# Performance work log

Measured on AMD Instinct MI355X. Metric: run time of the kernel, lower is better.

The kernel has to match this reference:

```python
import jax, jax.numpy as jnp
import numpy as np

B, T, C = 1, 2048, 2048
H = 16
DN, DR, DV = 128, 64, 128          # qk_nope_head_dim, qk_rope_head_dim, v_head_dim
QKD = DN + DR                      # 192
RQ, RKV = 1536, 512                # q_lora_rank, kv_lora_rank
EPS = 1e-6
SCALE = QKD ** -0.5


def rmsnorm(v, w):
    return v * jax.lax.rsqrt(jnp.mean(v * v, axis=-1, keepdims=True) + EPS) * w


def rope(x, freqs):
    # x: (B, T, H, d), freqs: (T, d//2) angles. Consecutive-pair complex rotation
    # matching torch view_as_complex(x.reshape(..., -1, 2)) * freqs.
    cos = jnp.cos(freqs)[None, :, None, :]
    sin = jnp.sin(freqs)[None, :, None, :]
    xp = x.reshape(*x.shape[:-1], -1, 2)
    xr, xi = xp[..., 0], xp[..., 1]
    outr = xr * cos - xi * sin
    outi = xr * sin + xi * cos
    return jnp.stack([outr, outi], axis=-1).reshape(x.shape)


def setup_inputs() -> dict:
    key = jax.random.key(0)
    ks = jax.random.split(key, 8)
    s = 0.02
    pos = jnp.arange(T, dtype=jnp.float32)
    inv = 1.0 / (10000.0 ** (jnp.arange(0, DR, 2, dtype=jnp.float32) / DR))  # (DR/2,)
    freqs = pos[:, None] * inv[None, :]  # (T, DR/2) rotation angles
    return {
        "x": jax.random.normal(ks[0], (B, T, C), jnp.float32),
        "freqs": freqs,
        "wq_a": jax.random.normal(ks[1], (RQ, C), jnp.float32) * s,
        "bq_a": jnp.zeros((RQ,), jnp.float32),
        "q_norm_w": jnp.ones((RQ,), jnp.float32),
        "wq_b": jax.random.normal(ks[2], (H * QKD, RQ), jnp.float32) * s,
        "bq_b": jnp.zeros((H * QKD,), jnp.float32),
        "wkv_a": jax.random.normal(ks[3], (RKV + DR, C), jnp.float32) * s,
        "bkv_a": jnp.zeros((RKV + DR,), jnp.float32),
        "kv_norm_w": jnp.ones((RKV,), jnp.float32),
        "wkv_b": jax.random.normal(ks[4], (H * (DN + DV), RKV), jnp.float32) * s,
        "bkv_b": jnp.zeros((H * (DN + DV),), jnp.float32),
        "wo": jax.random.normal(ks[5], (C, C), jnp.float32) * s,
        "bo": jnp.zeros((C,), jnp.float32),
        "prefill": 1,
        "cache_pos": 0,
    }


def reference(x, freqs, wq_a, bq_a, q_norm_w, wq_b, bq_b, wkv_a, bkv_a,
              kv_norm_w, wkv_b, bkv_b, wo, bo, prefill, cache_pos):
    # --- low-rank Q projection ---
    q_lat = rmsnorm(x @ wq_a.T + bq_a, q_norm_w)                 # (B,T,RQ)
    q = (q_lat @ wq_b.T + bq_b).reshape(B, T, H, QKD)
    q_nope, q_pe = q[..., :DN], q[..., DN:]
    q_pe = rope(q_pe, freqs)

    # --- low-rank KV projection ---
    kvpe = x @ wkv_a.T + bkv_a                                   # (B,T,RKV+DR)
    kv_lat, k_pe = kvpe[..., :RKV], kvpe[..., RKV:]
    k_pe = rope(k_pe[:, :, None, :], freqs)                      # (B,T,1,DR)
    kvb = (rmsnorm(kv_lat, kv_norm_w) @ wkv_b.T + bkv_b).reshape(B, T, H, DN + DV)
    k_nope, v = kvb[..., :DN], kvb[..., DN:]

    q = jnp.concatenate([q_nope, q_pe], axis=-1)                 # (B,T,H,QKD)
    k = jnp.concatenate([k_nope, jnp.broadcast_to(k_pe, (B, T, H, DR))], axis=-1)

    # --- causal SDPA (prefill: cache holds exactly the current T tokens) ---
    scores = jnp.einsum('bthd,bshd->bhts', q, k) * SCALE         # (B,H,T,T)
    mask = jnp.tril(jnp.ones((T, T), dtype=bool))
    scores = jnp.where(mask, scores, -jnp.inf)
    att = jax.nn.softmax(scores, axis=-1)
    y = jnp.einsum('bhts,bshd->bthd', att, v).reshape(B, T, C)
    return y @ wo.T + bo
```

## Files before the change

kernel.cpp:

```cpp
#include <hip/hip_runtime.h>
#include <hip/hip_bf16.h>


#define T_DIM 2048
#define H_DIM 16
#define SCALE_F 0.07216878364870322f
#define EPS_F 1e-6f
#define NEG_INF (-3.402823466e38f)

typedef __attribute__((ext_vector_type(8))) short short8;
typedef __attribute__((ext_vector_type(4))) float f32x4;
typedef __attribute__((address_space(3))) char lds_char;
typedef const __attribute__((address_space(1))) char glb_char;

__device__ inline void st_out(float* p, float v) { *p = v; }
__device__ inline void st_out(__hip_bfloat16* p, float v) { *p = __float2bfloat16(v); }

__global__ void cast_bf16_kernel(const float* __restrict__ src,
                                 __hip_bfloat16* __restrict__ dst,
                                 int n4_src, int n4_dst) {
    int i = blockIdx.x * 256 + threadIdx.x;
    if (i >= n4_dst) return;
    float4 v = make_float4(0.f, 0.f, 0.f, 0.f);
    if (i < n4_src) v = ((const float4*)src)[i];
    dst[4 * i + 0] = __float2bfloat16(v.x);
    dst[4 * i + 1] = __float2bfloat16(v.y);
    dst[4 * i + 2] = __float2bfloat16(v.z);
    dst[4 * i + 3] = __float2bfloat16(v.w);
}

__global__ void pad_bias_kernel(const float* __restrict__ src, float* __restrict__ dst,
                                int n_src, int n_dst) {
    int i = blockIdx.x * 256 + threadIdx.x;
    if (i < n_dst) dst[i] = (i < n_src) ? src[i] : 0.f;
}

template <typename OT>
__global__ __launch_bounds__(512) void gemm_mfma_kernel(
    const __hip_bfloat16* __restrict__ A, int lda,
    const __hip_bfloat16* __restrict__ W, int ldw,
    const float* __restrict__ bias,
    OT* __restrict__ C, int ldc,
    float* __restrict__ C2, int ldc2, int splitN, int K) {
    __shared__ __hip_bfloat16 As[2][128 * 32];
    __shared__ __hip_bfloat16 Bs[2][128 * 32];
    const int tid = threadIdx.x;
    const int w = tid >> 6, lane = tid & 63, qd = lane >> 4, lx = lane & 15;
    const int rowB = blockIdx.y * 128, colB = blockIdx.x * 128;
    const int wr = (w >> 1) * 32, wc = (w & 1) * 64;

    f32x4 acc[2][4];
#pragma unroll
    for (int i = 0; i < 2; ++i)
#pragma unroll
        for (int j = 0; j < 4; ++j) acc[i][j] = (f32x4)(0.f);

    auto stage = [&](int buf, int k0) {
        const int g = tid, row = g >> 2, q = g & 3;
        const __hip_bfloat16* ga = A + (size_t)(rowB + row) * lda + k0 + q * 8;
        __builtin_amdgcn_global_load_lds((glb_char*)ga,
            (lds_char*)((char*)&As[buf][0] + (size_t)g * 16), 16, 0, 0);
        const __hip_bfloat16* gb = W + (size_t)(colB + row) * ldw + k0 + q * 8;
        __builtin_amdgcn_global_load_lds((glb_char*)gb,
            (lds_char*)((char*)&Bs[buf][0] + (size_t)g * 16), 16, 0, 0);
    };

    stage(0, 0);
    __syncthreads();
    int cur = 0;
    for (int k0 = 0; k0 < K; k0 += 32) {
        if (k0 + 32 < K) stage(cur ^ 1, k0 + 32);

        short8 a[2], b[4];
#pragma unroll
        for (int rt = 0; rt < 2; ++rt)
            a[rt] = *(const short8*)&As[cur][(wr + rt * 16 + lx) * 32 + qd * 8];
#pragma unroll
        for (int ct = 0; ct < 4; ++ct)
            b[ct] = *(const short8*)&Bs[cur][(wc + ct * 16 + lx) * 32 + qd * 8];
#pragma unroll
        for (int rt = 0; rt < 2; ++rt)
#pragma unroll
            for (int ct = 0; ct < 4; ++ct)
                acc[rt][ct] = __builtin_amdgcn_mfma_f32_16x16x32_bf16(a[rt], b[ct], acc[rt][ct], 0, 0, 0);
        __syncthreads();
        cur ^= 1;
    }

    const bool second = (C2 != nullptr) && (colB >= splitN);
#pragma unroll
    for (int rt = 0; rt < 2; ++rt)
#pragma unroll
        for (int j = 0; j < 4; ++j) {
            const int row = rowB + wr + rt * 16 + 4 * qd + j;
#pragma unroll
            for (int ct = 0; ct < 4; ++ct) {
                const int col = colB + wc + ct * 16 + lx;
                const float v = acc[rt][ct][j] + bias[col];
                if (second) C2[(size_t)row * ldc2 + (col - splitN)] = v;
                else        st_out(&C[(size_t)row * ldc + col], v);
            }
        }
}

__global__ void rmsnorm_kernel(const float* __restrict__ in, __hip_bfloat16* __restrict__ outp,
                               const float* __restrict__ w,
                               int D, int in_stride, int out_stride) {
    const int row = blockIdx.x;
    const float* p = in + (size_t)row * in_stride;
    __hip_bfloat16* o = outp + (size_t)row * out_stride;
    const int tid = threadIdx.x;
    float ss = 0.f;
    for (int i = tid; i < D; i += 256) { float v = p[i]; ss += v * v; }
    __shared__ float red[256];
    red[tid] = ss;
    __syncthreads();
    for (int off = 128; off > 0; off >>= 1) {
        if (tid < off) red[tid] += red[tid + off];
        __syncthreads();
    }
    const float scale = rsqrtf(red[0] / (float)D + EPS_F);
    for (int i = tid; i < D; i += 256)
        o[i] = __float2bfloat16(p[i] * scale * w[i]);
}

__global__ void rope_q_bf_kernel(__hip_bfloat16* __restrict__ qb,
                                 const float* __restrict__ freqs) {
    const int idx = blockIdx.x * 256 + threadIdx.x;
    const int t = idx >> 9;
    const int h = (idx >> 5) & 15;
    const int i = idx & 31;
    const float f = freqs[t * 32 + i];
    const float c = cosf(f), s = sinf(f);
    __hip_bfloat16* p = qb + (size_t)t * 3072 + h * 192 + 128 + 2 * i;
    const float xr = __bfloat162float(p[0]), xi = __bfloat162float(p[1]);
    p[0] = __float2bfloat16(xr * c - xi * s);
    p[1] = __float2bfloat16(xr * s + xi * c);
}

__global__ void rope_k_bf_kernel(const float* __restrict__ kvpe,
                                 const float* __restrict__ freqs,
                                 __hip_bfloat16* __restrict__ kpe) {
    const int idx = blockIdx.x * 256 + threadIdx.x;
    const int t = idx >> 5;
    const int i = idx & 31;
    const float f = freqs[t * 32 + i];
    const float c = cosf(f), s = sinf(f);
    const float* src = kvpe + (size_t)t * 640 + 512 + 2 * i;
    const float xr = src[0], xi = src[1];
    kpe[(size_t)t * 64 + 2 * i]     = __float2bfloat16(xr * c - xi * s);
    kpe[(size_t)t * 64 + 2 * i + 1] = __float2bfloat16(xr * s + xi * c);
}

__global__ void pack_vT_kernel(const __hip_bfloat16* __restrict__ kvb,
                               __hip_bfloat16* __restrict__ vT) {
    const int t0 = blockIdx.x * 64;
    const int h = blockIdx.y;
    const int tid = threadIdx.x;
    __shared__ __hip_bfloat16 Ls[64][136];
#pragma unroll
    for (int it = 0; it < 4; ++it) {
        int c = tid + 256 * it;
        int i = c >> 4, part = c & 15;
        *(uint4*)&Ls[i][part * 8] =
            *(const uint4*)(kvb + (size_t)(t0 + i) * 4096 + h * 256 + 128 + part * 8);
    }
    __syncthreads();
#pragma unroll
    for (int it = 0; it < 32; ++it) {
        int c = tid + 256 * it;
        int d = c >> 6, i = c & 63;
        vT[((size_t)(h * 128 + d)) * 2048 + t0 + i] = Ls[i][d];
    }
}

__global__ __launch_bounds__(256) void attn_mfma_kernel(
    const __hip_bfloat16* __restrict__ q,
    const __hip_bfloat16* __restrict__ kv,
    const __hip_bfloat16* __restrict__ kpe,
    const __hip_bfloat16* __restrict__ vT,
    __hip_bfloat16* __restrict__ y) {
    const int qt = gridDim.x - 1 - blockIdx.x;
    const int h = blockIdx.y;
    const int q0 = qt * 64;
    const int tid = threadIdx.x;
    const int w = tid >> 6, lane = tid & 63, qd = lane >> 4, lx = lane & 15;

    __shared__ __hip_bfloat16 Ks[64][200];
    __shared__ __hip_bfloat16 Vs[128][72];
    __shared__ __hip_bfloat16 Ps[4][16][72];

    short8 qf[6];
    {
        const __hip_bfloat16* qrow =
            q + (size_t)(q0 + 16 * w + lx) * 3072 + h * 192 + qd * 8;
#pragma unroll
        for (int kc = 0; kc < 6; ++kc)
            qf[kc] = *(const short8*)(qrow + kc * 32);
    }

    f32x4 O[8];
#pragma unroll
    for (int i = 0; i < 8; ++i) O[i] = (f32x4)(0.f);
    float mrow[4], lrow[4];
#pragma unroll
    for (int j = 0; j < 4; ++j) { mrow[j] = NEG_INF; lrow[j] = 0.f; }

    const short8 vone = (short8)(short)0x3F80;

    uint4 k0r, k1r, k2r, k3r, pe0r, pe1r, v0r, v1r, v2r, v3r;
    const __hip_bfloat16* kvh = kv + h * 256;
    const __hip_bfloat16* vTh = vT + (size_t)h * 128 * 2048;

#define PREFETCH(S0)                                                               \
    do {                                                                           \
        const size_t kk_ = (size_t)(S0) + (tid >> 4);                              \
        const int kp_ = (tid & 15) * 8;                                            \
        k0r = *(const uint4*)(kvh + (kk_ +  0) * 4096 + kp_);                      \
        k1r = *(const uint4*)(kvh + (kk_ + 16) * 4096 + kp_);                      \
        k2r = *(const uint4*)(kvh + (kk_ + 32) * 4096 + kp_);                      \
        k3r = *(const uint4*)(kvh + (kk_ + 48) * 4096 + kp_);                      \
        const size_t pk_ = (size_t)(S0) + (tid >> 3);                              \
        const int pp_ = (tid & 7) * 8;                                             \
        pe0r = *(const uint4*)(kpe + (pk_ +  0) * 64 + pp_);                       \
        pe1r = *(const uint4*)(kpe + (pk_ + 32) * 64 + pp_);                       \
        const __hip_bfloat16* vp_ = vTh + ((size_t)(tid >> 3)) * 2048 + (S0) + pp_;\
        v0r = *(const uint4*)(vp_ + 0 * 65536);                                    \
        v1r = *(const uint4*)(vp_ + 1 * 65536);                                    \
        v2r = *(const uint4*)(vp_ + 2 * 65536);                                    \
        v3r = *(const uint4*)(vp_ + 3 * 65536);                                    \
    } while (0)

    PREFETCH(0);

    for (int s0 = 0; s0 <= q0 + 63; s0 += 64) {
        __syncthreads();
        {
            const int kr_ = tid >> 4, kp_ = (tid & 15) * 8;
            *(uint4*)&Ks[kr_ +  0][kp_] = k0r;
            *(uint4*)&Ks[kr_ + 16][kp_] = k1r;
            *(uint4*)&Ks[kr_ + 32][kp_] = k2r;
            *(uint4*)&Ks[kr_ + 48][kp_] = k3r;
            const int pr_ = tid >> 3, pp_ = (tid & 7) * 8;
            *(uint4*)&Ks[pr_ +  0][128 + pp_] = pe0r;
            *(uint4*)&Ks[pr_ + 32][128 + pp_] = pe1r;
            *(uint4*)&Vs[pr_ +  0][pp_] = v0r;
            *(uint4*)&Vs[pr_ + 32][pp_] = v1r;
            *(uint4*)&Vs[pr_ + 64][pp_] = v2r;
            *(uint4*)&Vs[pr_ + 96][pp_] = v3r;
        }
        __syncthreads();

        if (s0 + 64 <= q0) PREFETCH(s0 + 64);

        f32x4 S[4];
#pragma unroll
        for (int nt = 0; nt < 4; ++nt) S[nt] = (f32x4)(0.f);
        __builtin_amdgcn_s_setprio(1);
#pragma unroll
        for (int kc = 0; kc < 6; ++kc) {
            short8 a = qf[kc];
#pragma unroll
            for (int nt = 0; nt < 4; ++nt) {
                short8 b = *(const short8*)&Ks[nt * 16 + lx][kc * 32 + qd * 8];
                S[nt] = __builtin_amdgcn_mfma_f32_16x16x32_bf16(a, b, S[nt], 0, 0, 0);
            }
        }
        __builtin_amdgcn_s_setprio(0);

        float sv[4][4];
#pragma unroll
        for (int nt = 0; nt < 4; ++nt) {
            int col = s0 + nt * 16 + lx;
#pragma unroll
            for (int j = 0; j < 4; ++j) {
                int row = q0 + 16 * w + 4 * qd + j;
                float v = S[nt][j] * SCALE_F;
                sv[nt][j] = (col > row) ? NEG_INF : v;
            }
        }

        float mn[4], al[4];
#pragma unroll
        for (int j = 0; j < 4; ++j) {
            float rm = fmaxf(fmaxf(sv[0][j], sv[1][j]), fmaxf(sv[2][j], sv[3][j]));
#pragma unroll
            for (int msk = 1; msk < 16; msk <<= 1)
                rm = fmaxf(rm, __shfl_xor(rm, msk));
            mn[j] = fmaxf(mrow[j], rm);
            al[j] = __expf(mrow[j] - mn[j]);
            mrow[j] = mn[j];
        }
#pragma unroll
        for (int nt = 0; nt < 4; ++nt)
#pragma unroll
            for (int j = 0; j < 4; ++j) {
                float p = __expf(sv[nt][j] - mn[j]);
                Ps[w][4 * qd + j][nt * 16 + lx] = __float2bfloat16(p);
            }
#pragma unroll
        for (int nt = 0; nt < 8; ++nt)
#pragma unroll
            for (int j = 0; j < 4; ++j) O[nt][j] *= al[j];

        asm volatile("s_waitcnt lgkmcnt(0)" ::: "memory");

        f32x4 lacc = (f32x4)(0.f);
        __builtin_amdgcn_s_setprio(1);
#pragma unroll
        for (int kc2 = 0; kc2 < 2; ++kc2) {
            short8 pa = *(const short8*)&Ps[w][lx][kc2 * 32 + qd * 8];
#pragma unroll
            for (int nt = 0; nt < 8; ++nt) {
                short8 vb = *(const short8*)&Vs[nt * 16 + lx][kc2 * 32 + qd * 8];
                O[nt] = __builtin_amdgcn_mfma_f32_16x16x32_bf16(pa, vb, O[nt], 0, 0, 0);
            }
            lacc = __builtin_amdgcn_mfma_f32_16x16x32_bf16(pa, vone, lacc, 0, 0, 0);
        }
        __builtin_amdgcn_s_setprio(0);

#pragma unroll
        for (int j = 0; j < 4; ++j)
            lrow[j] = lrow[j] * al[j] + lacc[j];
    }
#undef PREFETCH

#pragma unroll
    for (int j = 0; j < 4; ++j) {
        const float inv = 1.f / lrow[j];
        const int t = q0 + 16 * w + 4 * qd + j;
        __hip_bfloat16* yr = y + (size_t)t * 2048 + h * 128 + lx;
#pragma unroll
        for (int nt = 0; nt < 8; ++nt) yr[nt * 16] = __float2bfloat16(O[nt][j] * inv);
    }
}

extern "C" void kernel_launch(void* const* d_in, const int* in_sizes, int n_in,
                              void* d_out, int out_size, void* d_ws, size_t ws_size,
                              hipStream_t stream) {
    const float* x         = (const float*)d_in[0];
    const float* freqs     = (const float*)d_in[1];
    const float* wq_a      = (const float*)d_in[2];
    const float* bq_a      = (const float*)d_in[3];
    const float* q_norm_w  = (const float*)d_in[4];
    const float* wq_b      = (const float*)d_in[5];
    const float* bq_b      = (const float*)d_in[6];
    const float* wkv_a     = (const float*)d_in[7];
    const float* bkv_a     = (const float*)d_in[8];
    const float* kv_norm_w = (const float*)d_in[9];
    const float* wkv_b     = (const float*)d_in[10];
    const float* bkv_b     = (const float*)d_in[11];
    const float* wo        = (const float*)d_in[12];
    const float* bo        = (const float*)d_in[13];
    float* out = (float*)d_out;

    char* p = (char*)d_ws;
    float* q_lat = (float*)p;                        p += (size_t)2048 * 1536 * 4;
    float* kvpe  = (float*)p;                        p += (size_t)2048 * 640 * 4;
    __hip_bfloat16* x_bf      = (__hip_bfloat16*)p;  p += (size_t)2048 * 2048 * 2;
    __hip_bfloat16* q_lat_bf  = (__hip_bfloat16*)p;  p += (size_t)2048 * 1536 * 2;
    __hip_bfloat16* qb_bf     = (__hip_bfloat16*)p;  p += (size_t)2048 * 3072 * 2;
    __hip_bfloat16* kv_lat_bf = (__hip_bfloat16*)p;  p += (size_t)2048 * 512 * 2;
    __hip_bfloat16* kvb_bf    = (__hip_bfloat16*)p;  p += (size_t)2048 * 4096 * 2;
    __hip_bfloat16* kpe_bf    = (__hip_bfloat16*)p;  p += (size_t)2048 * 64 * 2;
    __hip_bfloat16* WA        = (__hip_bfloat16*)p;  p += (size_t)3072 * 1536 * 2;
    float* bias_ab = (float*)p;                      p += (size_t)2176 * 4;
    __hip_bfloat16* vT    = x_bf;
    __hip_bfloat16* yb_bf = (__hip_bfloat16*)q_lat;

    cast_bf16_kernel<<<4096, 256, 0, stream>>>(x, x_bf, 1048576, 1048576);
    cast_bf16_kernel<<<3072, 256, 0, stream>>>(wq_a, WA, 786432, 786432);
    cast_bf16_kernel<<<1280, 256, 0, stream>>>(wkv_a, WA + (size_t)1536 * 2048, 294912, 327680);
    pad_bias_kernel<<<6, 256, 0, stream>>>(bq_a, bias_ab, 1536, 1536);
    pad_bias_kernel<<<3, 256, 0, stream>>>(bkv_a, bias_ab + 1536, 576, 640);
    gemm_mfma_kernel<float><<<dim3(17, 16), 512, 0, stream>>>(
        x_bf, 2048, WA, 2048, bias_ab, q_lat, 1536, kvpe, 640, 1536, 2048);
    rmsnorm_kernel<<<2048, 256, 0, stream>>>(q_lat, q_lat_bf, q_norm_w, 1536, 1536, 1536);
    cast_bf16_kernel<<<4608, 256, 0, stream>>>(wq_b, WA, 1179648, 1179648);
    gemm_mfma_kernel<__hip_bfloat16><<<dim3(24, 16), 512, 0, stream>>>(
        q_lat_bf, 1536, WA, 1536, bq_b, qb_bf, 3072, nullptr, 0, 1 << 30, 1536);
    rope_q_bf_kernel<<<4096, 256, 0, stream>>>(qb_bf, freqs);
    rope_k_bf_kernel<<<256, 256, 0, stream>>>(kvpe, freqs, kpe_bf);
    rmsnorm_kernel<<<2048, 256, 0, stream>>>(kvpe, kv_lat_bf, kv_norm_w, 512, 640, 512);
    cast_bf16_kernel<<<2048, 256, 0, stream>>>(wkv_b, WA, 524288, 524288);
    gemm_mfma_kernel<__hip_bfloat16><<<dim3(32, 16), 512, 0, stream>>>(
        kv_lat_bf, 512, WA, 512, bkv_b, kvb_bf, 4096, nullptr, 0, 1 << 30, 512);
    pack_vT_kernel<<<dim3(32, 16), 256, 0, stream>>>(kvb_bf, vT);
    attn_mfma_kernel<<<dim3(32, 16), 256, 0, stream>>>(qb_bf, kvb_bf, kpe_bf, vT, yb_bf);
    cast_bf16_kernel<<<4096, 256, 0, stream>>>(wo, WA, 1048576, 1048576);
    gemm_mfma_kernel<float><<<dim3(16, 16), 512, 0, stream>>>(
        yb_bf, 2048, WA, 2048, bo, out, 2048, nullptr, 0, 1 << 30, 2048);
}
```

Baseline: 396.6 us.

## Deepen GEMM K-tile with swizzled LDS, XCD-aware remap, lazy softmax rescale, fuse small kernels

The GEMM K-step grows from 32 to 64 with XOR-swizzled LDS staging to avoid bank conflicts, and workgroups are remapped so neighbouring tiles share an XCD's L2. The attention kernel swizzles its K/V LDS tiles, maps heads to XCDs, and skips the online-softmax rescale unless the running max grows by more than a threshold. Several small prep kernels (weight casts, bias pads, kv rmsnorm plus k rope) are merged to cut launch count. The changes raise LDS usage per GEMM block and make the softmax path approximate-stable via a fixed threshold.

```diff
diff --git a/kernel.cpp b/kernel.cpp
--- a/kernel.cpp
+++ b/kernel.cpp
@@ -29,10 +29,27 @@
     dst[4 * i + 3] = __float2bfloat16(v.w);
 }
 
-__global__ void pad_bias_kernel(const float* __restrict__ src, float* __restrict__ dst,
-                                int n_src, int n_dst) {
+__global__ void cast_wa_kernel(const float* __restrict__ wq_a,
+                               const float* __restrict__ wkv_a,
+                               __hip_bfloat16* __restrict__ WA) {
     int i = blockIdx.x * 256 + threadIdx.x;
-    if (i < n_dst) dst[i] = (i < n_src) ? src[i] : 0.f;
+    if (i >= 1114112) return;
+    float4 v = make_float4(0.f, 0.f, 0.f, 0.f);
+    if (i < 786432) v = ((const float4*)wq_a)[i];
+    else if (i - 786432 < 294912) v = ((const float4*)wkv_a)[i - 786432];
+    __hip_bfloat16* dst = WA + 4 * (size_t)i;
+    dst[0] = __float2bfloat16(v.x);
+    dst[1] = __float2bfloat16(v.y);
+    dst[2] = __float2bfloat16(v.z);
+    dst[3] = __float2bfloat16(v.w);
+}
+
+__global__ void bias_ab_kernel(const float* __restrict__ bq_a,
+                               const float* __restrict__ bkv_a,
+                               float* __restrict__ dst) {
+    int i = blockIdx.x * 256 + threadIdx.x;
+    if (i >= 2176) return;
+    dst[i] = (i < 1536) ? bq_a[i] : ((i - 1536) < 576 ? bkv_a[i - 1536] : 0.f);
 }
 
 template <typename OT>
@@ -42,11 +59,18 @@
     const float* __restrict__ bias,
     OT* __restrict__ C, int ldc,
     float* __restrict__ C2, int ldc2, int splitN, int K) {
-    __shared__ __hip_bfloat16 As[2][128 * 32];
-    __shared__ __hip_bfloat16 Bs[2][128 * 32];
+    __shared__ __hip_bfloat16 As[2][128 * 64];
+    __shared__ __hip_bfloat16 Bs[2][128 * 64];
     const int tid = threadIdx.x;
     const int w = tid >> 6, lane = tid & 63, qd = lane >> 4, lx = lane & 15;
-    const int rowB = blockIdx.y * 128, colB = blockIdx.x * 128;
+
+    const int nwg = gridDim.x * gridDim.y;
+    const int o = blockIdx.y * gridDim.x + blockIdx.x;
+    const int qx = nwg >> 3, rx = nwg & 7;
+    const int xcd = o & 7, idx = o >> 3;
+    const int neu = (xcd < rx ? xcd * (qx + 1) : rx * (qx + 1) + (xcd - rx) * qx) + idx;
+    const int rowB = (neu / gridDim.x) * 128, colB = (neu % gridDim.x) * 128;
+
     const int wr = (w >> 1) * 32, wc = (w & 1) * 64;
 
     f32x4 acc[2][4];
@@ -56,33 +80,44 @@
         for (int j = 0; j < 4; ++j) acc[i][j] = (f32x4)(0.f);
 
     auto stage = [&](int buf, int k0) {
-        const int g = tid, row = g >> 2, q = g & 3;
-        const __hip_bfloat16* ga = A + (size_t)(rowB + row) * lda + k0 + q * 8;
-        __builtin_amdgcn_global_load_lds((glb_char*)ga,
-            (lds_char*)((char*)&As[buf][0] + (size_t)g * 16), 16, 0, 0);
-        const __hip_bfloat16* gb = W + (size_t)(colB + row) * ldw + k0 + q * 8;
-        __builtin_amdgcn_global_load_lds((glb_char*)gb,
-            (lds_char*)((char*)&Bs[buf][0] + (size_t)g * 16), 16, 0, 0);
+#pragma unroll
+        for (int it = 0; it < 2; ++it) {
+            const int g = tid + it * 512;
+            const int row = g >> 3, s = g & 7;
+            const int sc = (s ^ (row & 7)) * 8;
+            const __hip_bfloat16* ga = A + (size_t)(rowB + row) * lda + k0 + sc;
+            __builtin_amdgcn_global_load_lds((glb_char*)ga,
+                (lds_char*)((char*)&As[buf][0] + (size_t)g * 16), 16, 0, 0);
+            const __hip_bfloat16* gb = W + (size_t)(colB + row) * ldw + k0 + sc;
+            __builtin_amdgcn_global_load_lds((glb_char*)gb,
+                (lds_char*)((char*)&Bs[buf][0] + (size_t)g * 16), 16, 0, 0);
+        }
     };
 
     stage(0, 0);
     __syncthreads();
     int cur = 0;
-    for (int k0 = 0; k0 < K; k0 += 32) {
-        if (k0 + 32 < K) stage(cur ^ 1, k0 + 32);
-
-        short8 a[2], b[4];
-#pragma unroll
-        for (int rt = 0; rt < 2; ++rt)
-            a[rt] = *(const short8*)&As[cur][(wr + rt * 16 + lx) * 32 + qd * 8];
-#pragma unroll
-        for (int ct = 0; ct < 4; ++ct)
-            b[ct] = *(const short8*)&Bs[cur][(wc + ct * 16 + lx) * 32 + qd * 8];
-#pragma unroll
-        for (int rt = 0; rt < 2; ++rt)
+    const int swz = (lx & 7) << 4;
+    for (int k0 = 0; k0 < K; k0 += 64) {
+        if (k0 + 64 < K) stage(cur ^ 1, k0 + 64);
+
+#pragma unroll
+        for (int kk = 0; kk < 2; ++kk) {
+            short8 a[2], b[4];
+#pragma unroll
+            for (int rt = 0; rt < 2; ++rt)
+                a[rt] = *(const short8*)((char*)&As[cur][0]
+                    + (size_t)(wr + rt * 16 + lx) * 128 + ((kk * 64 + qd * 16) ^ swz));
 #pragma unroll
             for (int ct = 0; ct < 4; ++ct)
-                acc[rt][ct] = __builtin_amdgcn_mfma_f32_16x16x32_bf16(a[rt], b[ct], acc[rt][ct], 0, 0, 0);
+                b[ct] = *(const short8*)((char*)&Bs[cur][0]
+                    + (size_t)(wc + ct * 16 + lx) * 128 + ((kk * 64 + qd * 16) ^ swz));
+#pragma unroll
+            for (int rt = 0; rt < 2; ++rt)
+#pragma unroll
+                for (int ct = 0; ct < 4; ++ct)
+                    acc[rt][ct] = __builtin_amdgcn_mfma_f32_16x16x32_bf16(a[rt], b[ct], acc[rt][ct], 0, 0, 0);
+        }
         __syncthreads();
         cur ^= 1;
     }
@@ -124,6 +159,35 @@
         o[i] = __float2bfloat16(p[i] * scale * w[i]);
 }
 
+__global__ void rmsnorm_rope_kv_kernel(const float* __restrict__ kvpe,
+                                       __hip_bfloat16* __restrict__ kv_lat_bf,
+                                       const float* __restrict__ w,
+                                       const float* __restrict__ freqs,
+                                       __hip_bfloat16* __restrict__ kpe) {
+    const int row = blockIdx.x;
+    const float* p = kvpe + (size_t)row * 640;
+    const int tid = threadIdx.x;
+    float v0 = p[tid], v1 = p[tid + 256];
+    __shared__ float red[256];
+    red[tid] = v0 * v0 + v1 * v1;
+    __syncthreads();
+    for (int off = 128; off > 0; off >>= 1) {
+        if (tid < off) red[tid] += red[tid + off];
+        __syncthreads();
+    }
+    const float scale = rsqrtf(red[0] / 512.f + EPS_F);
+    __hip_bfloat16* o = kv_lat_bf + (size_t)row * 512;
+    o[tid]       = __float2bfloat16(v0 * scale * w[tid]);
+    o[tid + 256] = __float2bfloat16(v1 * scale * w[tid + 256]);
+    if (tid < 32) {
+        const float f = freqs[row * 32 + tid];
+        const float c = cosf(f), s = sinf(f);
+        const float xr = p[512 + 2 * tid], xi = p[512 + 2 * tid + 1];
+        kpe[(size_t)row * 64 + 2 * tid]     = __float2bfloat16(xr * c - xi * s);
+        kpe[(size_t)row * 64 + 2 * tid + 1] = __float2bfloat16(xr * s + xi * c);
+    }
+}
+
 __global__ void rope_q_bf_kernel(__hip_bfloat16* __restrict__ qb,
                                  const float* __restrict__ freqs) {
     const int idx = blockIdx.x * 256 + threadIdx.x;
@@ -138,20 +202,6 @@
     p[1] = __float2bfloat16(xr * s + xi * c);
 }
 
-__global__ void rope_k_bf_kernel(const float* __restrict__ kvpe,
-                                 const float* __restrict__ freqs,
-                                 __hip_bfloat16* __restrict__ kpe) {
-    const int idx = blockIdx.x * 256 + threadIdx.x;
-    const int t = idx >> 5;
-    const int i = idx & 31;
-    const float f = freqs[t * 32 + i];
-    const float c = cosf(f), s = sinf(f);
-    const float* src = kvpe + (size_t)t * 640 + 512 + 2 * i;
-    const float xr = src[0], xi = src[1];
-    kpe[(size_t)t * 64 + 2 * i]     = __float2bfloat16(xr * c - xi * s);
-    kpe[(size_t)t * 64 + 2 * i + 1] = __float2bfloat16(xr * s + xi * c);
-}
-
 __global__ void pack_vT_kernel(const __hip_bfloat16* __restrict__ kvb,
                                __hip_bfloat16* __restrict__ vT) {
     const int t0 = blockIdx.x * 64;
@@ -180,15 +230,20 @@
     const __hip_bfloat16* __restrict__ kpe,
     const __hip_bfloat16* __restrict__ vT,
     __hip_bfloat16* __restrict__ y) {
-    const int qt = gridDim.x - 1 - blockIdx.x;
-    const int h = blockIdx.y;
+    const int o = blockIdx.x;
+    const int xcd = o & 7, slot = o >> 3;
+    const int h  = xcd * 2 + (slot & 1);
+    const int qt = 31 - (slot >> 1);
     const int q0 = qt * 64;
     const int tid = threadIdx.x;
     const int w = tid >> 6, lane = tid & 63, qd = lane >> 4, lx = lane & 15;
 
-    __shared__ __hip_bfloat16 Ks[64][200];
-    __shared__ __hip_bfloat16 Vs[128][72];
+    __shared__ __hip_bfloat16 KsB[64 * 192];
+    __shared__ __hip_bfloat16 VsB[128 * 64];
     __shared__ __hip_bfloat16 Ps[4][16][72];
+
+#define KS_ADDR(row, boff) ((char*)KsB + (size_t)(row) * 384 + ((boff) ^ (((row) & 7) << 4)))
+#define VS_ADDR(row, boff) ((char*)VsB + (size_t)(row) * 128 + ((boff) ^ (((row) & 7) << 4)))
 
     short8 qf[6];
     {
@@ -236,18 +291,18 @@
     for (int s0 = 0; s0 <= q0 + 63; s0 += 64) {
         __syncthreads();
         {
-            const int kr_ = tid >> 4, kp_ = (tid & 15) * 8;
-            *(uint4*)&Ks[kr_ +  0][kp_] = k0r;
-            *(uint4*)&Ks[kr_ + 16][kp_] = k1r;
-            *(uint4*)&Ks[kr_ + 32][kp_] = k2r;
-            *(uint4*)&Ks[kr_ + 48][kp_] = k3r;
-            const int pr_ = tid >> 3, pp_ = (tid & 7) * 8;
-            *(uint4*)&Ks[pr_ +  0][128 + pp_] = pe0r;
-            *(uint4*)&Ks[pr_ + 32][128 + pp_] = pe1r;
-            *(uint4*)&Vs[pr_ +  0][pp_] = v0r;
-            *(uint4*)&Vs[pr_ + 32][pp_] = v1r;
-            *(uint4*)&Vs[pr_ + 64][pp_] = v2r;
-            *(uint4*)&Vs[pr_ + 96][pp_] = v3r;
+            const int kr_ = tid >> 4, kb_ = (tid & 15) * 16;
+            *(uint4*)KS_ADDR(kr_ +  0, kb_) = k0r;
+            *(uint4*)KS_ADDR(kr_ + 16, kb_) = k1r;
+            *(uint4*)KS_ADDR(kr_ + 32, kb_) = k2r;
+            *(uint4*)KS_ADDR(kr_ + 48, kb_) = k3r;
+            const int pr_ = tid >> 3, pb_ = (tid & 7) * 16;
+            *(uint4*)KS_ADDR(pr_ +  0, 256 + pb_) = pe0r;
+            *(uint4*)KS_ADDR(pr_ + 32, 256 + pb_) = pe1r;
+            *(uint4*)VS_ADDR(pr_ +  0, pb_) = v0r;
+            *(uint4*)VS_ADDR(pr_ + 32, pb_) = v1r;
+            *(uint4*)VS_ADDR(pr_ + 64, pb_) = v2r;
+            *(uint4*)VS_ADDR(pr_ + 96, pb_) = v3r;
         }
         __syncthreads();
 
@@ -262,7 +317,7 @@
             short8 a = qf[kc];
 #pragma unroll
             for (int nt = 0; nt < 4; ++nt) {
-                short8 b = *(const short8*)&Ks[nt * 16 + lx][kc * 32 + qd * 8];
+                short8 b = *(const short8*)KS_ADDR(nt * 16 + lx, kc * 64 + qd * 16);
                 S[nt] = __builtin_amdgcn_mfma_f32_16x16x32_bf16(a, b, S[nt], 0, 0, 0);
             }
         }
@@ -280,28 +335,39 @@
             }
         }
 
-        float mn[4], al[4];
-#pragma unroll
-        for (int j = 0; j < 4; ++j) {
-            float rm = fmaxf(fmaxf(sv[0][j], sv[1][j]), fmaxf(sv[2][j], sv[3][j]));
-#pragma unroll
-            for (int msk = 1; msk < 16; msk <<= 1)
-                rm = fmaxf(rm, __shfl_xor(rm, msk));
-            mn[j] = fmaxf(mrow[j], rm);
-            al[j] = __expf(mrow[j] - mn[j]);
-            mrow[j] = mn[j];
+        float pmax[4];
+#pragma unroll
+        for (int j = 0; j < 4; ++j)
+            pmax[j] = fmaxf(fmaxf(sv[0][j], sv[1][j]), fmaxf(sv[2][j], sv[3][j]));
+        const bool need = !__all((pmax[0] <= mrow[0] + 8.f) &&
+                                 (pmax[1] <= mrow[1] + 8.f) &&
+                                 (pmax[2] <= mrow[2] + 8.f) &&
+                                 (pmax[3] <= mrow[3] + 8.f));
+        if (need) {
+            float al[4];
+#pragma unroll
+            for (int j = 0; j < 4; ++j) {
+                float rm = pmax[j];
+#pragma unroll
+                for (int msk = 1; msk < 16; msk <<= 1)
+                    rm = fmaxf(rm, __shfl_xor(rm, msk));
+                const float mn = fmaxf(mrow[j], rm);
+                al[j] = __expf(mrow[j] - mn);
+                mrow[j] = mn;
+                lrow[j] *= al[j];
+            }
+#pragma unroll
+            for (int nt = 0; nt < 8; ++nt)
+#pragma unroll
+                for (int j = 0; j < 4; ++j) O[nt][j] *= al[j];
         }
 #pragma unroll
         for (int nt = 0; nt < 4; ++nt)
 #pragma unroll
             for (int j = 0; j < 4; ++j) {
-                float p = __expf(sv[nt][j] - mn[j]);
+                float p = __expf(sv[nt][j] - mrow[j]);
                 Ps[w][4 * qd + j][nt * 16 + lx] = __float2bfloat16(p);
             }
-#pragma unroll
-        for (int nt = 0; nt < 8; ++nt)
-#pragma unroll
-            for (int j = 0; j < 4; ++j) O[nt][j] *= al[j];
 
         asm volatile("s_waitcnt lgkmcnt(0)" ::: "memory");
 
@@ -312,7 +378,7 @@
             short8 pa = *(const short8*)&Ps[w][lx][kc2 * 32 + qd * 8];
 #pragma unroll
             for (int nt = 0; nt < 8; ++nt) {
-                short8 vb = *(const short8*)&Vs[nt * 16 + lx][kc2 * 32 + qd * 8];
+                short8 vb = *(const short8*)VS_ADDR(nt * 16 + lx, kc2 * 64 + qd * 16);
                 O[nt] = __builtin_amdgcn_mfma_f32_16x16x32_bf16(pa, vb, O[nt], 0, 0, 0);
             }
             lacc = __builtin_amdgcn_mfma_f32_16x16x32_bf16(pa, vone, lacc, 0, 0, 0);
@@ -320,10 +386,11 @@
         __builtin_amdgcn_s_setprio(0);
 
 #pragma unroll
-        for (int j = 0; j < 4; ++j)
-            lrow[j] = lrow[j] * al[j] + lacc[j];
+        for (int j = 0; j < 4; ++j) lrow[j] += lacc[j];
     }
 #undef PREFETCH
+#undef KS_ADDR
+#undef VS_ADDR
 
 #pragma unroll
     for (int j = 0; j < 4; ++j) {
@@ -369,10 +436,8 @@
     __hip_bfloat16* yb_bf = (__hip_bfloat16*)q_lat;
 
     cast_bf16_kernel<<<4096, 256, 0, stream>>>(x, x_bf, 1048576, 1048576);
-    cast_bf16_kernel<<<3072, 256, 0, stream>>>(wq_a, WA, 786432, 786432);
-    cast_bf16_kernel<<<1280, 256, 0, stream>>>(wkv_a, WA + (size_t)1536 * 2048, 294912, 327680);
-    pad_bias_kernel<<<6, 256, 0, stream>>>(bq_a, bias_ab, 1536, 1536);
-    pad_bias_kernel<<<3, 256, 0, stream>>>(bkv_a, bias_ab + 1536, 576, 640);
+    cast_wa_kernel<<<4352, 256, 0, stream>>>(wq_a, wkv_a, WA);
+    bias_ab_kernel<<<9, 256, 0, stream>>>(bq_a, bkv_a, bias_ab);
     gemm_mfma_kernel<float><<<dim3(17, 16), 512, 0, stream>>>(
         x_bf, 2048, WA, 2048, bias_ab, q_lat, 1536, kvpe, 640, 1536, 2048);
     rmsnorm_kernel<<<2048, 256, 0, stream>>>(q_lat, q_lat_bf, q_norm_w, 1536, 1536, 1536);
@@ -380,13 +445,12 @@
     gemm_mfma_kernel<__hip_bfloat16><<<dim3(24, 16), 512, 0, stream>>>(
         q_lat_bf, 1536, WA, 1536, bq_b, qb_bf, 3072, nullptr, 0, 1 << 30, 1536);
     rope_q_bf_kernel<<<4096, 256, 0, stream>>>(qb_bf, freqs);
-    rope_k_bf_kernel<<<256, 256, 0, stream>>>(kvpe, freqs, kpe_bf);
-    rmsnorm_kernel<<<2048, 256, 0, stream>>>(kvpe, kv_lat_bf, kv_norm_w, 512, 640, 512);
+    rmsnorm_rope_kv_kernel<<<2048, 256, 0, stream>>>(kvpe, kv_lat_bf, kv_norm_w, freqs, kpe_bf);
     cast_bf16_kernel<<<2048, 256, 0, stream>>>(wkv_b, WA, 524288, 524288);
     gemm_mfma_kernel<__hip_bfloat16><<<dim3(32, 16), 512, 0, stream>>>(
         kv_lat_bf, 512, WA, 512, bkv_b, kvb_bf, 4096, nullptr, 0, 1 << 30, 512);
     pack_vT_kernel<<<dim3(32, 16), 256, 0, stream>>>(kvb_bf, vT);
-    attn_mfma_kernel<<<dim3(32, 16), 256, 0, stream>>>(qb_bf, kvb_bf, kpe_bf, vT, yb_bf);
+    attn_mfma_kernel<<<512, 256, 0, stream>>>(qb_bf, kvb_bf, kpe_bf, vT, yb_bf);
     cast_bf16_kernel<<<4096, 256, 0, stream>>>(wo, WA, 1048576, 1048576);
     gemm_mfma_kernel<float><<<dim3(16, 16), 512, 0, stream>>>(
         yb_bf, 2048, WA, 2048, bo, out, 2048, nullptr, 0, 1 << 30, 2048);
```

Result: faster. 346.1 us (-12.7%).
